# Performance work log

Measured on AMD Instinct MI355X. Metric: run time of the kernel, lower is better.

The kernel has to match this reference:

```python
import jax, jax.numpy as jnp
import numpy as np

B, S, D, H = 2, 2048, 1024, 16
DK = D // H  # 64
THETA = 10000.0


def _rope_tables(seq_len, d_k, theta):
    pos = jnp.arange(seq_len, dtype=jnp.float32)  # [S]
    dim = jnp.arange(0, d_k, 2, dtype=jnp.float32)  # [DK/2]
    inv_freq = 1.0 / theta ** (dim / d_k)
    angle = pos[:, None] * inv_freq[None, :]  # [S, DK/2]
    angle = jnp.repeat(angle, 2, axis=-1)  # repeat_interleave -> [S, DK]
    return jnp.cos(angle), jnp.sin(angle)


def _apply_rope(x, cos, sin):
    # x: [..., S, DK]; interleaved pair rotation
    x1 = x[..., ::2]
    x2 = x[..., 1::2]
    x_perm = jnp.stack([-x2, x1], axis=-1).reshape(x.shape)
    return x * cos + x_perm * sin


def setup_inputs() -> dict:
    key = jax.random.key(0)
    ks = jax.random.split(key, 5)
    std = np.sqrt(2.0 / (D + D)).astype(np.float32)
    return {
        "x": jax.random.normal(ks[0], (B, S, D), dtype=jnp.float32),
        "Wq": jax.random.normal(ks[1], (D, D), dtype=jnp.float32) * std,
        "Wk": jax.random.normal(ks[2], (D, D), dtype=jnp.float32) * std,
        "Wv": jax.random.normal(ks[3], (D, D), dtype=jnp.float32) * std,
        "Wo": jax.random.normal(ks[4], (D, D), dtype=jnp.float32) * std,
    }


def reference(x, Wq, Wk, Wv, Wo):
    seq_len = x.shape[-2]
    # projections: weight is [d_out, d_in], applied as x @ W^T
    def split_heads(t):
        return t.reshape(*t.shape[:-1], H, DK).swapaxes(-3, -2)  # [B, H, S, DK]

    Q = split_heads(jnp.einsum('bsd,od->bso', x, Wq))
    K = split_heads(jnp.einsum('bsd,od->bso', x, Wk))
    V = split_heads(jnp.einsum('bsd,od->bso', x, Wv))

    cos, sin = _rope_tables(seq_len, DK, THETA)  # [S, DK]
    Q = _apply_rope(Q, cos, sin)
    K = _apply_rope(K, cos, sin)

    scale = 1.0 / np.sqrt(DK).astype(np.float32)
    logits = jnp.einsum('bhnd,bhmd->bhnm', Q, K) * scale  # [B, H, S, S]
    causal = jnp.tril(jnp.ones((seq_len, seq_len), dtype=bool))
    logits = jnp.where(causal, logits, -jnp.inf)
    probs = jax.nn.softmax(logits, axis=-1)
    attn = jnp.einsum('bhnm,bhmd->bhnd', probs, V)  # [B, H, S, DK]
    attn = attn.swapaxes(-3, -2).reshape(*x.shape[:-1], D)  # [B, S, D]
    return jnp.einsum('bsd,od->bso', attn, Wo)
```

## Files before the change

### kernel.cpp

```cpp
#include <hip/hip_runtime.h>
#include <hip/hip_bf16.h>
#include <cstdint>
#include <cstddef>

#define BB 2
#define SS 2048
#define DD 1024
#define HH 16
#define DKK 64
#define MM (BB*SS)

typedef __bf16 bf16x8 __attribute__((ext_vector_type(8)));
typedef float  f32x4  __attribute__((ext_vector_type(4)));

__device__ __forceinline__ unsigned short f2bf(float f) {
    unsigned u = __float_as_uint(f);
    u += 0x7FFF + ((u >> 16) & 1);
    return (unsigned short)(u >> 16);
}

#if __has_builtin(__builtin_amdgcn_cvt_pk_bf16_f32)
typedef __bf16 bf16v2 __attribute__((ext_vector_type(2)));
__device__ __forceinline__ unsigned pk_bf16(float a, float b) {
    bf16v2 v = __builtin_amdgcn_cvt_pk_bf16_f32(a, b);
    return __builtin_bit_cast(unsigned, v);
}
#else
__device__ __forceinline__ unsigned pk_bf16(float a, float b) {
    return (unsigned)f2bf(a) | ((unsigned)f2bf(b) << 16);
}
#endif

__device__ __forceinline__ void gld_lds16(const void* g, void* l) {
    __builtin_amdgcn_global_load_lds(
        (const __attribute__((address_space(1))) unsigned int*)g,
        (__attribute__((address_space(3))) unsigned int*)l, 16, 0, 0);
}

#define WAIT_VM8() __builtin_amdgcn_s_waitcnt(0x0F78)
#define WAIT_VM4() __builtin_amdgcn_s_waitcnt(0x0F74)
#define WAIT_VM3() __builtin_amdgcn_s_waitcnt(0x0F73)
#define WAIT_VM0() __builtin_amdgcn_s_waitcnt(0x0F70)
#define BARRIER()  __builtin_amdgcn_s_barrier()

__global__ __launch_bounds__(256) void cast_all(const float* __restrict__ x,
                                                const float* __restrict__ wq,
                                                const float* __restrict__ wk,
                                                const float* __restrict__ wv,
                                                const float* __restrict__ wo,
                                                unsigned short* __restrict__ xb,
                                                unsigned short* __restrict__ wb) {
    int i = (blockIdx.x * 256 + threadIdx.x) * 4;
    const float* src;
    unsigned short* dst;
    if (i < MM * DD) { src = x + i; dst = xb + i; }
    else {
        int e = i - MM * DD;
        int r = e >> 20;
        const float* s0 = (r == 0) ? wq : (r == 1) ? wk : (r == 2) ? wv : wo;
        src = s0 + (e & ((1 << 20) - 1));
        dst = wb + e;
    }
    float4 v = *reinterpret_cast<const float4*>(src);
    ushort4 o;
    o.x = f2bf(v.x); o.y = f2bf(v.y); o.z = f2bf(v.z); o.w = f2bf(v.w);
    *reinterpret_cast<ushort4*>(dst) = o;
}

__global__ __launch_bounds__(256, 3) void gemm_qkv(const unsigned short* __restrict__ A,
                                                   const unsigned short* __restrict__ W,
                                                   unsigned short* __restrict__ Qo,
                                                   unsigned short* __restrict__ Ko,
                                                   unsigned short* __restrict__ Vto) {
    __shared__ __align__(16) unsigned short A0[128 * 32], W0[128 * 32];
    __shared__ __align__(16) unsigned short A1[128 * 32], W1[128 * 32];
    const int tid  = threadIdx.x;
    const int wave = tid >> 6, lane = tid & 63;
    const int quad = lane >> 4, l16 = lane & 15;
    const int wm = wave >> 1, wn = wave & 1;
    const int m0 = blockIdx.y * 128, n0 = blockIdx.x * 128;
    const int sw3 = l16 & 3;

    f32x4 acc[4][4];
    for (int i = 0; i < 4; i++)
        for (int j = 0; j < 4; j++) acc[i][j] = f32x4{0.f, 0.f, 0.f, 0.f};

    auto stage = [&](int k0, unsigned short* As, unsigned short* Ws) {
        for (int c = tid; c < 512; c += 256) {
            int row = c >> 2, g = c & 3;
            int gc = ((g ^ (row & 3)) << 3);
            gld_lds16(A + (size_t)(m0 + row) * DD + k0 + gc, As + c * 8);
            gld_lds16(W + (size_t)(n0 + row) * DD + k0 + gc, Ws + c * 8);
        }
    };
    auto compute = [&](const unsigned short* As, const unsigned short* Ws) {
        bf16x8 af[4], bfb[4];
        for (int i = 0; i < 4; i++)
            af[i] = *reinterpret_cast<const bf16x8*>(As + (wm * 64 + i * 16 + l16) * 32 + ((quad ^ sw3) << 3));
        for (int j = 0; j < 4; j++)
            bfb[j] = *reinterpret_cast<const bf16x8*>(Ws + (wn * 64 + j * 16 + l16) * 32 + ((quad ^ sw3) << 3));
        for (int i = 0; i < 4; i++)
            for (int j = 0; j < 4; j++)
                acc[i][j] = __builtin_amdgcn_mfma_f32_16x16x32_bf16(af[i], bfb[j], acc[i][j], 0, 0, 0);
    };

    stage(0, A0, W0);
    int k0 = 0;
    while (true) {
        BARRIER();
        if (k0 + 32 < DD) { stage(k0 + 32, A1, W1); WAIT_VM4(); } else WAIT_VM0();
        BARRIER();
        compute(A0, W0);
        k0 += 32; if (k0 >= DD) break;

        BARRIER();
        if (k0 + 32 < DD) { stage(k0 + 32, A0, W0); WAIT_VM4(); } else WAIT_VM0();
        BARRIER();
        compute(A1, W1);
        k0 += 32; if (k0 >= DD) break;
    }

    const int region = n0 >> 10;
    const float L2T_OVER_DK = 13.287712379549449f / 64.0f;
    if (region < 2) {
        unsigned short* Co = region ? Ko : Qo;
        const float osc = (region == 0) ? 0.18033688011112042f : 1.0f;
        for (int i = 0; i < 4; i++) {
            int mrow = m0 + wm * 64 + i * 16 + quad * 4;
            int b = mrow >> 11, s0 = mrow & 2047;
            for (int j = 0; j < 4; j++) {
                int nc = (n0 + wn * 64 + j * 16 + l16) & 1023;
                int h = nc >> 6, dk = nc & 63;
                float inv_freq = exp2f(-(float)(dk & ~1) * L2T_OVER_DK);
                for (int r = 0; r < 4; r++) {
                    float v = acc[i][j][r];
                    float partner = __shfl_xor(v, 1, 64);
                    float sn, cs;
                    __sincosf((float)(s0 + r) * inv_freq, &sn, &cs);
                    float outv = (v * cs + ((dk & 1) ? partner : -partner) * sn) * osc;
                    Co[((size_t)(b * HH + h) * SS + (s0 + r)) * DKK + dk] = f2bf(outv);
                }
            }
        }
    } else {
        __syncthreads();
        unsigned short* T = A0 + wave * 1024;
        const int dkl = lane >> 2, s4 = (lane & 3) * 4;
        for (int i = 0; i < 4; i++) {
            int ms0 = m0 + wm * 64 + i * 16;
            for (int j = 0; j < 4; j++) {
                int nc0 = n0 + wn * 64 + j * 16;
                for (int r = 0; r < 4; r++)
                    T[(quad * 4 + r) * 17 + l16] = f2bf(acc[i][j][r]);
                ushort4 o;
                o.x = T[(s4 + 0) * 17 + dkl];
                o.y = T[(s4 + 1) * 17 + dkl];
                o.z = T[(s4 + 2) * 17 + dkl];
                o.w = T[(s4 + 3) * 17 + dkl];
                int nc = (nc0 + dkl) & 1023;
                int h = nc >> 6, dk = nc & 63;
                int m = ms0 + s4;
                int b = m >> 11, s = m & 2047;
                *reinterpret_cast<ushort4*>(Vto + ((size_t)((b * HH + h) * DKK + dk)) * SS + s) = o;
            }
        }
    }
}

__global__ __launch_bounds__(256, 3) void gemm_out(const unsigned short* __restrict__ A,
                                                   const unsigned short* __restrict__ W,
                                                   float* __restrict__ C) {
    __shared__ __align__(16) unsigned short A0[64 * 32], W0[128 * 32];
    __shared__ __align__(16) unsigned short A1[64 * 32], W1[128 * 32];
    const int tid  = threadIdx.x;
    const int wave = tid >> 6, lane = tid & 63;
    const int quad = lane >> 4, l16 = lane & 15;
    const int wm = wave >> 1, wn = wave & 1;
    const int m0 = blockIdx.y * 64, n0 = blockIdx.x * 128;
    const int sw3 = l16 & 3;

    f32x4 acc[2][4];
    for (int i = 0; i < 2; i++)
        for (int j = 0; j < 4; j++) acc[i][j] = f32x4{0.f, 0.f, 0.f, 0.f};

    auto stage = [&](int k0, unsigned short* As, unsigned short* Ws) {
        {
            int row = tid >> 2, g = tid & 3;
            int gc = ((g ^ (row & 3)) << 3);
            gld_lds16(A + (size_t)(m0 + row) * DD + k0 + gc, As + tid * 8);
        }
        for (int c = tid; c < 512; c += 256) {
            int row = c >> 2, g = c & 3;
            int gc = ((g ^ (row & 3)) << 3);
            gld_lds16(W + (size_t)(n0 + row) * DD + k0 + gc, Ws + c * 8);
        }
    };
    auto compute = [&](const unsigned short* As, const unsigned short* Ws) {
        bf16x8 af[2], bfb[4];
        for (int i = 0; i < 2; i++)
            af[i] = *reinterpret_cast<const bf16x8*>(As + (wm * 32 + i * 16 + l16) * 32 + ((quad ^ sw3) << 3));
        for (int j = 0; j < 4; j++)
            bfb[j] = *reinterpret_cast<const bf16x8*>(Ws + (wn * 64 + j * 16 + l16) * 32 + ((quad ^ sw3) << 3));
        for (int i = 0; i < 2; i++)
            for (int j = 0; j < 4; j++)
                acc[i][j] = __builtin_amdgcn_mfma_f32_16x16x32_bf16(af[i], bfb[j], acc[i][j], 0, 0, 0);
    };

    stage(0, A0, W0);
    int k0 = 0;
    while (true) {
        BARRIER();
        if (k0 + 32 < DD) { stage(k0 + 32, A1, W1); WAIT_VM3(); } else WAIT_VM0();
        BARRIER();
        compute(A0, W0);
        k0 += 32; if (k0 >= DD) break;

        BARRIER();
        if (k0 + 32 < DD) { stage(k0 + 32, A0, W0); WAIT_VM3(); } else WAIT_VM0();
        BARRIER();
        compute(A1, W1);
        k0 += 32; if (k0 >= DD) break;
    }

    for (int i = 0; i < 2; i++) {
        int mrow = m0 + wm * 32 + i * 16 + quad * 4;
        for (int j = 0; j < 4; j++) {
            int ncol = n0 + wn * 64 + j * 16 + l16;
            for (int r = 0; r < 4; r++)
                C[(size_t)(mrow + r) * DD + ncol] = acc[i][j][r];
        }
    }
}

__global__ __launch_bounds__(256, 3) void attn_kernel(const unsigned short* __restrict__ Qb,
                                                      const unsigned short* __restrict__ Kb,
                                                      const unsigned short* __restrict__ Vtb,
                                                      unsigned short* __restrict__ attn) {
    __shared__ __align__(16) unsigned short K0s[64 * 64], V0s[64 * 64];
    __shared__ __align__(16) unsigned short K1s[64 * 64], V1s[64 * 64];
    __shared__ __align__(16) unsigned short Ps[4][16 * 72];

    const int tid  = threadIdx.x;
    const int wave = tid >> 6, lane = tid & 63;
    const int quad = lane >> 4, l16 = lane & 15;

    const int lin = blockIdx.x;
    const int xcd = lin & 7, idx = lin >> 3;
    const int bh  = xcd * 4 + (idx & 3);
    const int tau = 31 - (idx >> 2);
    const int nST = tau + 1;

    const int swK = l16 & 7;
    const int q0r = tau * 64;

    const unsigned short* Qg = Qb  + (size_t)bh * SS * DKK;
    const unsigned short* Kg = Kb  + (size_t)bh * SS * DKK;
    const unsigned short* Vg = Vtb + (size_t)bh * DKK * SS;

    bf16x8 q0 = *reinterpret_cast<const bf16x8*>(Qg + (size_t)(q0r + wave * 16 + l16) * DKK + quad * 8);
    bf16x8 q1 = *reinterpret_cast<const bf16x8*>(Qg + (size_t)(q0r + wave * 16 + l16) * DKK + 32 + quad * 8);

    bf16x8 vone;
    for (int tt = 0; tt < 8; tt++) vone[tt] = (__bf16)1.0f;

    f32x4 ao[4], al;
    for (int j = 0; j < 4; j++) ao[j] = f32x4{0.f,0.f,0.f,0.f};
    al = f32x4{0.f,0.f,0.f,0.f};

    auto stage = [&](int s, unsigned short* Kd, unsigned short* Vd) {
        const int kv0 = s * 64;
        for (int c = tid; c < 512; c += 256) {
            int rowK = c >> 3, gK = c & 7;
            gld_lds16(Kg + (size_t)(kv0 + rowK) * DKK + ((gK ^ (rowK & 7)) << 3), Kd + c * 8);
            int rowV = c >> 3, gV = c & 7;
            gld_lds16(Vg + (size_t)rowV * SS + kv0 + ((gV ^ (rowV & 7)) << 3), Vd + c * 8);
        }
    };

    auto do_tile = [&](const unsigned short* Kd, const unsigned short* Vd, bool diag) {
        f32x4 sc[4];
        __builtin_amdgcn_s_setprio(1);
        for (int j = 0; j < 4; j++) {
            const unsigned short* kr = Kd + (j * 16 + l16) * 64;
            bf16x8 kf0 = *reinterpret_cast<const bf16x8*>(kr + ((quad ^ swK) << 3));
            bf16x8 kf1 = *reinterpret_cast<const bf16x8*>(kr + (((4 + quad) ^ swK) << 3));
            f32x4 s = f32x4{0.f, 0.f, 0.f, 0.f};
            s = __builtin_amdgcn_mfma_f32_16x16x32_bf16(kf0, q0, s, 0, 0, 0);
            s = __builtin_amdgcn_mfma_f32_16x16x32_bf16(kf1, q1, s, 0, 0, 0);
            sc[j] = s;
        }
        __builtin_amdgcn_s_setprio(0);
        if (diag) {
            int ql = wave * 16 + l16;
            for (int j = 0; j < 4; j++)
                for (int r = 0; r < 4; r++) {
                    int kvl = j * 16 + quad * 4 + r;
                    if (kvl > ql) sc[j][r] = -1e30f;
                }
        }
        for (int j = 0; j < 4; j++)
            for (int r = 0; r < 4; r++)
                sc[j][r] = exp2f(sc[j][r]);

        unsigned short* Pw = Ps[wave];
        for (int j = 0; j < 4; j++) {
            uint2 w;
            w.x = pk_bf16(sc[j][0], sc[j][1]);
            w.y = pk_bf16(sc[j][2], sc[j][3]);
            *reinterpret_cast<uint2*>(Pw + l16 * 72 + j * 16 + quad * 4) = w;
        }

        __builtin_amdgcn_s_setprio(1);
        for (int ko = 0; ko < 64; ko += 32) {
            bf16x8 pf = *reinterpret_cast<const bf16x8*>(Pw + l16 * 72 + ko + quad * 8);
            al = __builtin_amdgcn_mfma_f32_16x16x32_bf16(pf, vone, al, 0, 0, 0);
            int gg = (ko >> 3) + quad;
            for (int j = 0; j < 4; j++) {
                bf16x8 vf = *reinterpret_cast<const bf16x8*>(Vd + (j * 16 + l16) * 64 + ((gg ^ (l16 & 7)) << 3));
                ao[j] = __builtin_amdgcn_mfma_f32_16x16x32_bf16(pf, vf, ao[j], 0, 0, 0);
            }
        }
        __builtin_amdgcn_s_setprio(0);
    };

    stage(0, K0s, V0s);
    int s = 0;
    while (true) {
        BARRIER();
        if (s + 1 < nST) { stage(s + 1, K1s, V1s); WAIT_VM4(); } else WAIT_VM0();
        BARRIER();
        do_tile(K0s, V0s, s == tau);
        if (++s >= nST) break;

        BARRIER();
        if (s + 1 < nST) { stage(s + 1, K0s, V0s); WAIT_VM4(); } else WAIT_VM0();
        BARRIER();
        do_tile(K1s, V1s, s == tau);
        if (++s >= nST) break;
    }

    const int b = bh >> 4, h = bh & 15;
    for (int r = 0; r < 4; r++) {
        float invL = __builtin_amdgcn_rcpf(al[r]);
        int sr = q0r + wave * 16 + quad * 4 + r;
        for (int j = 0; j < 4; j++)
            attn[((size_t)(b * SS + sr)) * DD + h * DKK + j * 16 + l16] = f2bf(ao[j][r] * invL);
    }
}

extern "C" void kernel_launch(void* const* d_in, const int* in_sizes, int n_in,
                              void* d_out, int out_size, void* d_ws, size_t ws_size,
                              hipStream_t stream) {
    const float* x  = (const float*)d_in[0];
    const float* Wq = (const float*)d_in[1];
    const float* Wk = (const float*)d_in[2];
    const float* Wv = (const float*)d_in[3];
    const float* Wo = (const float*)d_in[4];

    char* ws = (char*)d_ws;
    const size_t MB = 1u << 20;
    unsigned short* xb    = (unsigned short*)(ws);
    unsigned short* wb    = (unsigned short*)(ws + 8  * MB);
    unsigned short* Qbuf  = (unsigned short*)(ws + 16 * MB);
    unsigned short* Kbuf  = (unsigned short*)(ws + 24 * MB);
    unsigned short* Vtbuf = (unsigned short*)(ws + 32 * MB);
    unsigned short* attnb = xb;

    cast_all<<<8192, 256, 0, stream>>>(x, Wq, Wk, Wv, Wo, xb, wb);

    gemm_qkv<<<dim3(24, 32), 256, 0, stream>>>(xb, wb, Qbuf, Kbuf, Vtbuf);

    attn_kernel<<<dim3(1024), 256, 0, stream>>>(Qbuf, Kbuf, Vtbuf, attnb);

    gemm_out<<<dim3(8, 64), 256, 0, stream>>>(attnb, wb + 3 * 1024 * 1024, (float*)d_out);
}
```

Baseline: 177.2 us.

## Keep P in registers via 16x16x16 MFMA, drop LDS round-trip

The attention kernel no longer writes the exponentiated scores P to shared memory and reads them back. Each lane's S-accumulator fragment is packed to bf16 and fed directly as the A operand of 16x16x16 bf16 MFMAs, whose operand layout matches the score accumulator layout, with the V fragment addressing changed to suit. Removing the per-wave P buffer also frees LDS, and the occupancy hint is raised from 3 to 4 blocks. The trade is twice as many MFMA instructions with half the K depth each, plus more, smaller LDS reads of V.

New measurement: 179.9 us. No clear change (+1.5%).

```diff
diff --git a/kernel.cpp b/kernel.cpp
--- a/kernel.cpp
+++ b/kernel.cpp
@@ -12,6 +12,7 @@
 
 typedef __bf16 bf16x8 __attribute__((ext_vector_type(8)));
 typedef float  f32x4  __attribute__((ext_vector_type(4)));
+typedef short  s16x4  __attribute__((ext_vector_type(4)));
 
 __device__ __forceinline__ unsigned short f2bf(float f) {
     unsigned u = __float_as_uint(f);
@@ -30,6 +31,17 @@
     return (unsigned)f2bf(a) | ((unsigned)f2bf(b) << 16);
 }
 #endif
+
+__device__ __forceinline__ f32x4 mfma16(s16x4 a, s16x4 b, f32x4 c) {
+#if __has_builtin(__builtin_amdgcn_mfma_f32_16x16x16bf16_1k)
+    return __builtin_amdgcn_mfma_f32_16x16x16bf16_1k(a, b, c, 0, 0, 0);
+#else
+    f32x4 d;
+    asm volatile("v_mfma_f32_16x16x16_bf16 %0, %1, %2, %3"
+                 : "=&v"(d) : "v"(a), "v"(b), "v"(c));
+    return d;
+#endif
+}
 
 __device__ __forceinline__ void gld_lds16(const void* g, void* l) {
     __builtin_amdgcn_global_load_lds(
@@ -232,13 +244,12 @@
     }
 }
 
-__global__ __launch_bounds__(256, 3) void attn_kernel(const unsigned short* __restrict__ Qb,
+__global__ __launch_bounds__(256, 4) void attn_kernel(const unsigned short* __restrict__ Qb,
                                                       const unsigned short* __restrict__ Kb,
                                                       const unsigned short* __restrict__ Vtb,
                                                       unsigned short* __restrict__ attn) {
     __shared__ __align__(16) unsigned short K0s[64 * 64], V0s[64 * 64];
     __shared__ __align__(16) unsigned short K1s[64 * 64], V1s[64 * 64];
-    __shared__ __align__(16) unsigned short Ps[4][16 * 72];
 
     const int tid  = threadIdx.x;
     const int wave = tid >> 6, lane = tid & 63;
@@ -260,8 +271,8 @@
     bf16x8 q0 = *reinterpret_cast<const bf16x8*>(Qg + (size_t)(q0r + wave * 16 + l16) * DKK + quad * 8);
     bf16x8 q1 = *reinterpret_cast<const bf16x8*>(Qg + (size_t)(q0r + wave * 16 + l16) * DKK + 32 + quad * 8);
 
-    bf16x8 vone;
-    for (int tt = 0; tt < 8; tt++) vone[tt] = (__bf16)1.0f;
+    uint2 uv1; uv1.x = 0x3F803F80u; uv1.y = 0x3F803F80u;
+    const s16x4 vone4 = __builtin_bit_cast(s16x4, uv1);
 
     f32x4 ao[4], al;
     for (int j = 0; j < 4; j++) ao[j] = f32x4{0.f,0.f,0.f,0.f};
@@ -302,22 +313,22 @@
             for (int r = 0; r < 4; r++)
                 sc[j][r] = exp2f(sc[j][r]);
 
-        unsigned short* Pw = Ps[wave];
+        s16x4 p[4];
         for (int j = 0; j < 4; j++) {
-            uint2 w;
-            w.x = pk_bf16(sc[j][0], sc[j][1]);
-            w.y = pk_bf16(sc[j][2], sc[j][3]);
-            *reinterpret_cast<uint2*>(Pw + l16 * 72 + j * 16 + quad * 4) = w;
+            uint2 u;
+            u.x = pk_bf16(sc[j][0], sc[j][1]);
+            u.y = pk_bf16(sc[j][2], sc[j][3]);
+            p[j] = __builtin_bit_cast(s16x4, u);
         }
 
         __builtin_amdgcn_s_setprio(1);
-        for (int ko = 0; ko < 64; ko += 32) {
-            bf16x8 pf = *reinterpret_cast<const bf16x8*>(Pw + l16 * 72 + ko + quad * 8);
-            al = __builtin_amdgcn_mfma_f32_16x16x32_bf16(pf, vone, al, 0, 0, 0);
-            int gg = (ko >> 3) + quad;
-            for (int j = 0; j < 4; j++) {
-                bf16x8 vf = *reinterpret_cast<const bf16x8*>(Vd + (j * 16 + l16) * 64 + ((gg ^ (l16 & 7)) << 3));
-                ao[j] = __builtin_amdgcn_mfma_f32_16x16x32_bf16(pf, vf, ao[j], 0, 0, 0);
+        for (int j = 0; j < 4; j++)
+            al = mfma16(p[j], vone4, al);
+        for (int j = 0; j < 4; j++) {
+            const int goff = (((2 * j + (quad >> 1)) ^ (l16 & 7)) << 3) + ((quad & 1) << 2);
+            for (int dkb = 0; dkb < 4; dkb++) {
+                s16x4 vf = *reinterpret_cast<const s16x4*>(Vd + ((dkb * 16 + l16) << 6) + goff);
+                ao[dkb] = mfma16(p[j], vf, ao[dkb]);
             }
         }
         __builtin_amdgcn_s_setprio(0);
```
